# Kernel tuning notes

Measured on AMD Instinct MI355X. Metric: run time of the kernel, lower is better.

Reference implementation:

```python
import jax, jax.numpy as jnp
import numpy as np

B, T = 2, 1000
IN_DIM, OUT_DIM = 257, 514
D_MODEL, D_STATE, D_CONV, EXPAND = 512, 16, 4, 2
D_INNER = EXPAND * D_MODEL          # 1024
DT_RANK = (D_MODEL + 15) // 16      # ceil(512/16) = 32
N_LAYER = 4
K_DC = 31                            # depthwise conv kernel in MambaDCLayer


def layer_norm(x, g, b, eps=1e-5):
    mu = jnp.mean(x, axis=-1, keepdims=True)
    var = jnp.mean((x - mu) ** 2, axis=-1, keepdims=True)
    return (x - mu) * jax.lax.rsqrt(var + eps) * g + b


def dw_conv1d(x, w, b, pad):
    # x: (B, T, C), w: (C, K) depthwise, pad: (left, right)
    y = jax.lax.conv_general_dilated(
        x.transpose(0, 2, 1), w[:, None, :], (1,), [pad],
        dimension_numbers=('NCH', 'OIH', 'NCH'), feature_group_count=w.shape[0])
    return (y + b[None, :, None]).transpose(0, 2, 1)


def mamba_block(x, W_in, conv_w, conv_b, W_x, W_dt, b_dt, A_log, Dp, W_out):
    # x: (B, T, d_model)
    xz = x @ W_in                               # (B, T, 2*D_INNER)
    xin, z = jnp.split(xz, 2, axis=-1)
    xin = dw_conv1d(xin, conv_w, conv_b, (D_CONV - 1, 0))  # causal depthwise conv
    xin = jax.nn.silu(xin)                      # (B, T, D_INNER)
    proj = xin @ W_x                            # (B, T, DT_RANK + 2*D_STATE)
    dt = jax.nn.softplus(proj[..., :DT_RANK] @ W_dt + b_dt)  # (B, T, D_INNER)
    Bm = proj[..., DT_RANK:DT_RANK + D_STATE]   # (B, T, D_STATE)
    Cm = proj[..., DT_RANK + D_STATE:]          # (B, T, D_STATE)
    A = -jnp.exp(A_log)                         # (D_INNER, D_STATE)
    dA = jnp.exp(dt[..., None] * A)             # (B, T, D_INNER, D_STATE)
    dBu = (dt * xin)[..., None] * Bm[:, :, None, :]  # (B, T, D_INNER, D_STATE)

    def step(h, inp):
        dA_t, dBu_t, C_t = inp
        h = dA_t * h + dBu_t
        return h, jnp.einsum('bds,bs->bd', h, C_t)

    h0 = jnp.zeros((x.shape[0], D_INNER, D_STATE), x.dtype)
    _, ys = jax.lax.scan(step, h0, (dA.transpose(1, 0, 2, 3),
                                    dBu.transpose(1, 0, 2, 3),
                                    Cm.transpose(1, 0, 2)))
    y = ys.transpose(1, 0, 2) + xin * Dp        # (B, T, D_INNER)
    y = y * jax.nn.silu(z)
    return y @ W_out                            # (B, T, d_model)


def setup_inputs() -> dict:
    key = jax.random.key(0)
    ks = iter(jax.random.split(key, 32))
    n = lambda shape, s=0.02: jax.random.normal(next(ks), shape, jnp.float32) * s
    return {
        'x': jax.random.normal(next(ks), (B, T, IN_DIM), jnp.float32),
        'lengths': jnp.full((B,), T, jnp.int32),
        'w_in0': n((IN_DIM, D_MODEL)),
        'ln_in_g': jnp.ones((D_MODEL,), jnp.float32),
        'ln_in_b': jnp.zeros((D_MODEL,), jnp.float32),
        'ln1_g': jnp.ones((N_LAYER, D_MODEL), jnp.float32),
        'ln1_b': jnp.zeros((N_LAYER, D_MODEL), jnp.float32),
        'W_inproj': n((N_LAYER, D_MODEL, 2 * D_INNER)),
        'conv_w': n((N_LAYER, D_INNER, D_CONV), 0.1),
        'conv_b': jnp.zeros((N_LAYER, D_INNER), jnp.float32),
        'W_xproj': n((N_LAYER, D_INNER, DT_RANK + 2 * D_STATE)),
        'W_dt': n((N_LAYER, DT_RANK, D_INNER), 0.1),
        'b_dt': jnp.full((N_LAYER, D_INNER), -4.6, jnp.float32),
        'A_log': jnp.tile(jnp.log(jnp.arange(1, D_STATE + 1, dtype=jnp.float32)),
                          (N_LAYER, D_INNER, 1)),
        'D': jnp.ones((N_LAYER, D_INNER), jnp.float32),
        'W_mo': n((N_LAYER, D_INNER, D_MODEL)),
        'ln2_g': jnp.ones((N_LAYER, D_MODEL), jnp.float32),
        'ln2_b': jnp.zeros((N_LAYER, D_MODEL), jnp.float32),
        'dc_w': n((N_LAYER, D_MODEL, K_DC), 0.1),
        'dc_b': jnp.zeros((N_LAYER, D_MODEL), jnp.float32),
        'w_out': n((D_MODEL, OUT_DIM)),
        'b_out': jnp.zeros((OUT_DIM,), jnp.float32),
    }


def reference(x, lengths, w_in0, ln_in_g, ln_in_b, ln1_g, ln1_b, W_inproj,
              conv_w, conv_b, W_xproj, W_dt, b_dt, A_log, D, W_mo,
              ln2_g, ln2_b, dc_w, dc_b, w_out, b_out):
    seq_mask = jnp.arange(x.shape[1]) < lengths[:, None]  # (B, T) bool
    h = jax.nn.relu(layer_norm(x @ w_in0, ln_in_g, ln_in_b))
    for i in range(N_LAYER):
        a = h + mamba_block(layer_norm(h, ln1_g[i], ln1_b[i]),
                            W_inproj[i], conv_w[i], conv_b[i], W_xproj[i],
                            W_dt[i], b_dt[i], A_log[i], D[i], W_mo[i])
        c = dw_conv1d(layer_norm(a, ln2_g[i], ln2_b[i]), dc_w[i], dc_b[i],
                      (K_DC // 2, K_DC // 2))  # 'same' padding
        h = a + c
    out = h @ w_out + b_out  # MagcIRM -> linear output head
    # lengths == T so output[seq_mask] is a full flatten to (B*T, OUT_DIM)
    out_flat = out.reshape(-1, out.shape[-1])
    return out_flat, seq_mask
```

## Files before the change

kernel.cpp:

```cpp
#include <hip/hip_runtime.h>
#include <cstdint>
#include <cstddef>

#define DEVI static __device__ __forceinline__

typedef unsigned short ushort_t;
typedef __attribute__((ext_vector_type(8))) short short8;
typedef __attribute__((ext_vector_type(4))) float f32x4;

DEVI float sp_softplus(float x) { return x > 20.f ? x : log1pf(__expf(x)); }
DEVI float silu_f(float x)      { return x / (1.f + __expf(-x)); }

DEVI ushort_t f2b(float v) {
    uint32_t u = __builtin_bit_cast(uint32_t, v);
    u += 0x7FFFu + ((u >> 16) & 1u);
    return (ushort_t)(u >> 16);
}
DEVI float b2f(ushort_t u) {
    uint32_t x = ((uint32_t)u) << 16;
    return __builtin_bit_cast(float, x);
}

DEVI void gload16(const ushort_t* g, ushort_t* l) {
    __builtin_amdgcn_global_load_lds(
        (const __attribute__((address_space(1))) unsigned int*)g,
        (__attribute__((address_space(3))) unsigned int*)l, 16, 0, 0);
}

#define NC 40
#define CL 25

template<bool RELU, bool OUTB16>
__global__ __launch_bounds__(256) void ln_k(const float* __restrict__ x,
                                            const float* __restrict__ g,
                                            const float* __restrict__ b,
                                            void* __restrict__ yv, int M)
{
    int wid  = threadIdx.x >> 6;
    int lane = threadIdx.x & 63;
    int row  = blockIdx.x * 4 + wid;
    if (row >= M) return;
    const float* xr = x + (size_t)row * 512;
    float4 v0 = *(const float4*)(xr + lane * 8);
    float4 v1 = *(const float4*)(xr + lane * 8 + 4);
    float vals[8] = {v0.x, v0.y, v0.z, v0.w, v1.x, v1.y, v1.z, v1.w};
    float s = 0.f;
#pragma unroll
    for (int i = 0; i < 8; i++) s += vals[i];
#pragma unroll
    for (int off = 1; off < 64; off <<= 1) s += __shfl_xor(s, off);
    float mu = s * (1.f / 512.f);
    float q = 0.f;
#pragma unroll
    for (int i = 0; i < 8; i++) { float d = vals[i] - mu; q += d * d; }
#pragma unroll
    for (int off = 1; off < 64; off <<= 1) q += __shfl_xor(q, off);
    float rstd = rsqrtf(q * (1.f / 512.f) + 1e-5f);
#pragma unroll
    for (int i = 0; i < 8; i++) {
        int c = lane * 8 + i;
        float o = (vals[i] - mu) * rstd * g[c] + b[c];
        if (RELU) o = fmaxf(o, 0.f);
        if (OUTB16) ((ushort_t*)yv)[(size_t)row * 512 + c] = f2b(o);
        else        ((float*)yv)[(size_t)row * 512 + c] = o;
    }
}

__global__ __launch_bounds__(256) void prep_all_k(const float* __restrict__ conv_w,
                                                  const float* __restrict__ dc_w,
                                                  const float* __restrict__ x,
                                                  float* __restrict__ cwt,
                                                  float* __restrict__ dcwt,
                                                  ushort_t* __restrict__ xb)
{
    int e = blockIdx.x * 256 + threadIdx.x;
    if (e < 16384) {
        int l = e >> 12, rem = e & 4095, k = rem >> 10, d = rem & 1023;
        cwt[e] = conv_w[l * 4096 + d * 4 + k];
        return;
    }
    e -= 16384;
    if (e < 63488) {
        int l = e / 15872, rem = e % 15872, k = rem / 512, m = rem % 512;
        dcwt[e] = dc_w[l * 15872 + m * 31 + k];
        return;
    }
    e -= 63488;
    if (e < 2000 * 320) {
        int k = e % 320, row = e / 320;
        xb[e] = (k < 257) ? f2b(x[(size_t)row * 257 + k]) : (ushort_t)0;
    }
}

__global__ __launch_bounds__(256) void tr_w_k(const float* __restrict__ src,
                                              ushort_t* __restrict__ dst,
                                              int Ktrue, int N, int ldo, int srcld,
                                              size_t sstride, size_t dstride)
{
    __shared__ float tile[32][33];
    src += blockIdx.z * sstride;
    dst += blockIdx.z * dstride;
    int n0 = blockIdx.x * 32, k0 = blockIdx.y * 32;
    int tx = threadIdx.x & 31, ty = threadIdx.x >> 5;
#pragma unroll
    for (int r = 0; r < 4; r++) {
        int k = k0 + ty + r * 8, n = n0 + tx;
        tile[ty + r * 8][tx] = (k < Ktrue && n < N) ? src[(size_t)k * srcld + n] : 0.f;
    }
    __syncthreads();
#pragma unroll
    for (int r = 0; r < 4; r++) {
        int n = n0 + ty + r * 8;
        if (n < N) dst[(size_t)n * ldo + k0 + tx] = f2b(tile[tx][ty + r * 8]);
    }
}

template<bool BIAS, int ACT, bool RES, bool OUTF32, bool OUTB16>
__global__ __launch_bounds__(256) void gemm7(
    const ushort_t* __restrict__ A, int lda,
    const ushort_t* __restrict__ Bt, int ldb,
    const float* __restrict__ bias,
    const float* __restrict__ R, int ldr,
    float* __restrict__ C, int ldc,
    ushort_t* __restrict__ C2, int ldc2,
    int M, int N, int K,
    size_t aStr, size_t bStr, size_t cStr)
{
    __shared__ ushort_t As[3 * 4096];
    __shared__ ushort_t Bs[3 * 4096];
    A  += blockIdx.z * aStr;
    Bt += blockIdx.z * bStr;
    C  += blockIdx.z * cStr;
    C2 += blockIdx.z * cStr;

    int tid = threadIdx.x;
    int wid = tid >> 6, l = tid & 63;
    int wr = wid >> 1, wc = wid & 1;
    int lk = l >> 4, lr = l & 15;
    int rhalf = tid >> 3, oct = tid & 7;

    int nwg = gridDim.x * gridDim.y;
    int bid = blockIdx.y * gridDim.x + blockIdx.x;
    {
        int q = nwg >> 3, r = nwg & 7;
        int xcd = bid & 7, lo = bid >> 3;
        bid = (xcd < r ? xcd * (q + 1) : r * (q + 1) + (xcd - r) * q) + lo;
    }
    int bx = bid % gridDim.x, by = bid / gridDim.x;
    int bm = by * 64, bn = bx * 64;

    int cg = oct ^ (rhalf & 7);
    const ushort_t* aS0 = A  + (size_t)(bm + rhalf) * lda + cg * 8;
    const ushort_t* aS1 = aS0 + (size_t)32 * lda;
    const ushort_t* bS0 = Bt + (size_t)(bn + rhalf) * ldb + cg * 8;
    const ushort_t* bS1 = bS0 + (size_t)32 * ldb;

    int rowA = wr * 32 + lr;
    int colB = wc * 32 + lr;
    int a0 = rowA * 64 + ((0 + lk) ^ (rowA & 7)) * 8;
    int a1 = rowA * 64 + ((4 + lk) ^ (rowA & 7)) * 8;
    int b0 = colB * 64 + ((0 + lk) ^ (colB & 7)) * 8;
    int b1 = colB * 64 + ((4 + lk) ^ (colB & 7)) * 8;

    f32x4 acc00 = {0.f,0.f,0.f,0.f}, acc01 = {0.f,0.f,0.f,0.f};
    f32x4 acc10 = {0.f,0.f,0.f,0.f}, acc11 = {0.f,0.f,0.f,0.f};

#define STAGE(B_) do { \
        gload16(aS0, &As[(B_) * 4096 + tid * 8]); \
        gload16(aS1, &As[(B_) * 4096 + 2048 + tid * 8]); \
        gload16(bS0, &Bs[(B_) * 4096 + tid * 8]); \
        gload16(bS1, &Bs[(B_) * 4096 + 2048 + tid * 8]); \
        aS0 += 64; aS1 += 64; bS0 += 64; bS1 += 64; \
    } while (0)

#define COMPUTE(B_) do { \
        short8 af0 = *(const short8*)&As[(B_) * 4096 + a0]; \
        short8 af1 = *(const short8*)&As[(B_) * 4096 + 1024 + a0]; \
        short8 bf0 = *(const short8*)&Bs[(B_) * 4096 + b0]; \
        short8 bf1 = *(const short8*)&Bs[(B_) * 4096 + 1024 + b0]; \
        acc00 = __builtin_amdgcn_mfma_f32_16x16x32_bf16(af0, bf0, acc00, 0, 0, 0); \
        acc01 = __builtin_amdgcn_mfma_f32_16x16x32_bf16(af0, bf1, acc01, 0, 0, 0); \
        acc10 = __builtin_amdgcn_mfma_f32_16x16x32_bf16(af1, bf0, acc10, 0, 0, 0); \
        acc11 = __builtin_amdgcn_mfma_f32_16x16x32_bf16(af1, bf1, acc11, 0, 0, 0); \
        af0 = *(const short8*)&As[(B_) * 4096 + a1]; \
        af1 = *(const short8*)&As[(B_) * 4096 + 1024 + a1]; \
        bf0 = *(const short8*)&Bs[(B_) * 4096 + b1]; \
        bf1 = *(const short8*)&Bs[(B_) * 4096 + 1024 + b1]; \
        acc00 = __builtin_amdgcn_mfma_f32_16x16x32_bf16(af0, bf0, acc00, 0, 0, 0); \
        acc01 = __builtin_amdgcn_mfma_f32_16x16x32_bf16(af0, bf1, acc01, 0, 0, 0); \
        acc10 = __builtin_amdgcn_mfma_f32_16x16x32_bf16(af1, bf0, acc10, 0, 0, 0); \
        acc11 = __builtin_amdgcn_mfma_f32_16x16x32_bf16(af1, bf1, acc11, 0, 0, 0); \
    } while (0)

#define STEP(T_, B_) do { \
        if ((T_) + 1 < nt) asm volatile("s_waitcnt vmcnt(4)" ::: "memory"); \
        else               asm volatile("s_waitcnt vmcnt(0)" ::: "memory"); \
        __builtin_amdgcn_s_barrier(); \
        if ((T_) + 2 < nt) STAGE(((B_) + 2) % 3); \
        COMPUTE(B_); \
    } while (0)

    int nt = K >> 6;
    STAGE(0);
    if (nt > 1) STAGE(1);
    int t = 0;
    for (; t + 3 <= nt; t += 3) { STEP(t, 0); STEP(t + 1, 1); STEP(t + 2, 2); }
    if (t < nt) { STEP(t, 0); t++; }
    if (t < nt) { STEP(t, 1); }

#undef STAGE
#undef COMPUTE
#undef STEP

    f32x4 accs[2][2] = {{acc00, acc01}, {acc10, acc11}};
#pragma unroll
    for (int m = 0; m < 2; m++) {
#pragma unroll
        for (int n = 0; n < 2; n++) {
            int gn = bn + wc * 32 + n * 16 + lr;
            if (gn >= N) continue;
#pragma unroll
            for (int r = 0; r < 4; r++) {
                int gm = bm + wr * 32 + m * 16 + lk * 4 + r;
                if (gm >= M) continue;
                float v = accs[m][n][r];
                if (ACT == 3) {
                    if (gn < 32) C2[(size_t)gm * ldc2 + gn] = f2b(v);
                    else { C[(size_t)gm * ldc + gn] = v;
                           C2[(size_t)gm * ldc2 + gn] = 0; }
                    continue;
                }
                if (BIAS) v += bias[gn];
                if (ACT == 1) v = sp_softplus(v);
                if (RES) v += R[(size_t)gm * ldr + gn];
                if (OUTF32) C[(size_t)gm * ldc + gn] = v;
                if (OUTB16) C2[(size_t)gm * ldc2 + gn] = f2b(v);
            }
        }
    }
}

__global__ __launch_bounds__(256) void conv4_silu_k(const ushort_t* __restrict__ xzb,
                                                    const float* __restrict__ cwt,
                                                    const float* __restrict__ bias,
                                                    ushort_t* __restrict__ xinb)
{
    int e = blockIdx.x * 256 + threadIdx.x;
    if (e >= 2000 * 128) return;
    int dg = (e & 127) * 8;
    int row = e >> 7;
    int b = row >= 1000 ? 1 : 0;
    int t = row - b * 1000;
    float acc[8];
#pragma unroll
    for (int j = 0; j < 8; j++) acc[j] = bias[dg + j];
#pragma unroll
    for (int k = 0; k < 4; k++) {
        int tt = t - 3 + k;
        if (tt < 0) continue;
        short8 v = *(const short8*)&xzb[(size_t)(b * 1000 + tt) * 2048 + dg];
#pragma unroll
        for (int j = 0; j < 8; j++)
            acc[j] += b2f((ushort_t)v[j]) * cwt[k * 1024 + dg + j];
    }
    short8 o;
#pragma unroll
    for (int j = 0; j < 8; j++) o[j] = (short)f2b(silu_f(acc[j]));
    *(short8*)&xinb[(size_t)row * 1024 + dg] = o;
}

__global__ __launch_bounds__(256) void scan_part1(const ushort_t* __restrict__ dt,
                                                  const ushort_t* __restrict__ xin,
                                                  const float* __restrict__ proj,
                                                  const float* __restrict__ A_log,
                                                  float* __restrict__ hloc,
                                                  float* __restrict__ sc)
{
    __shared__ ushort_t s_dt[CL][64], s_x[CL][64];
    __shared__ float s_B[CL][16];
    int d0 = blockIdx.x * 64;
    int c  = blockIdx.y;
    int b  = blockIdx.z;
    int tid = threadIdx.x;
    int ch = tid >> 2, st4 = tid & 3;
    int d = d0 + ch;
    int base = b * 1000 + c * CL;
    for (int lin = tid; lin < CL * 8; lin += 256) {
        int r = lin >> 3, q = lin & 7;
        size_t row = (size_t)(base + r);
        *(short8*)&s_dt[r][q * 8] = *(const short8*)&dt[row * 1024 + d0 + q * 8];
        *(short8*)&s_x[r][q * 8]  = *(const short8*)&xin[row * 1024 + d0 + q * 8];
    }
    for (int lin = tid; lin < CL * 16; lin += 256) {
        int r = lin >> 4, j = lin & 15;
        s_B[r][j] = proj[(size_t)(base + r) * 64 + 32 + j];
    }
    float4 alog = *(const float4*)&A_log[d * 16 + st4 * 4];
    float a_s[4] = {-__expf(alog.x), -__expf(alog.y), -__expf(alog.z), -__expf(alog.w)};
    __syncthreads();
    float h[4] = {0.f, 0.f, 0.f, 0.f};
    float sdt = 0.f;
#pragma unroll 5
    for (int t = 0; t < CL; t++) {
        float dtv = b2f(s_dt[t][ch]);
        float xv  = b2f(s_x[t][ch]);
        float4 Bv = *(const float4*)&s_B[t][st4 * 4];
        float dx = dtv * xv;
        sdt += dtv;
        h[0] = __expf(dtv * a_s[0]) * h[0] + dx * Bv.x;
        h[1] = __expf(dtv * a_s[1]) * h[1] + dx * Bv.y;
        h[2] = __expf(dtv * a_s[2]) * h[2] + dx * Bv.z;
        h[3] = __expf(dtv * a_s[3]) * h[3] + dx * Bv.w;
    }
    *(float4*)&hloc[((size_t)(b * NC + c) << 14) + ((size_t)d << 4) + st4 * 4] =
        (float4){h[0], h[1], h[2], h[3]};
    if (st4 == 0) sc[(b * NC + c) * 1024 + d] = sdt;
}

__global__ __launch_bounds__(256) void scan_combine(const float* __restrict__ A_log,
                                                    float* __restrict__ hloc,
                                                    const float* __restrict__ sc)
{
    int e = blockIdx.x * 256 + threadIdx.x;
    if (e >= 2 * 16384) return;
    int b = e >> 14;
    int rem = e & 16383;
    int dd = rem >> 4;
    float a_s = -__expf(A_log[rem]);
    float H = hloc[((size_t)(b * NC) << 14) + rem];
    for (int c = 1; c < NC; c++) {
        size_t idx = ((size_t)(b * NC + c) << 14) + rem;
        H = hloc[idx] + __expf(a_s * sc[(b * NC + c) * 1024 + dd]) * H;
        hloc[idx] = H;
    }
}

__global__ __launch_bounds__(256) void scan_part2(const ushort_t* __restrict__ dt,
                                                  const ushort_t* __restrict__ xin,
                                                  const float* __restrict__ proj,
                                                  const float* __restrict__ A_log,
                                                  const float* __restrict__ hend,
                                                  const float* __restrict__ Dp,
                                                  const ushort_t* __restrict__ xzb,
                                                  ushort_t* __restrict__ ysb)
{
    __shared__ ushort_t s_dt[CL][64], s_x[CL][64], s_y[CL][64];
    __shared__ float s_B[CL][16], s_C[CL][16];
    __shared__ float s_Dp[64];
    int d0 = blockIdx.x * 64;
    int c  = blockIdx.y;
    int b  = blockIdx.z;
    int tid = threadIdx.x;
    int ch = tid >> 2, st4 = tid & 3;
    int d = d0 + ch;
    int base = b * 1000 + c * CL;
    if (tid < 64) s_Dp[tid] = Dp[d0 + tid];
    for (int lin = tid; lin < CL * 8; lin += 256) {
        int r = lin >> 3, q = lin & 7;
        size_t row = (size_t)(base + r);
        *(short8*)&s_dt[r][q * 8] = *(const short8*)&dt[row * 1024 + d0 + q * 8];
        *(short8*)&s_x[r][q * 8]  = *(const short8*)&xin[row * 1024 + d0 + q * 8];
    }
    for (int lin = tid; lin < CL * 16; lin += 256) {
        int r = lin >> 4, j = lin & 15;
        s_B[r][j] = proj[(size_t)(base + r) * 64 + 32 + j];
        s_C[r][j] = proj[(size_t)(base + r) * 64 + 48 + j];
    }
    float4 alog = *(const float4*)&A_log[d * 16 + st4 * 4];
    float a_s[4] = {-__expf(alog.x), -__expf(alog.y), -__expf(alog.z), -__expf(alog.w)};
    float h[4] = {0.f, 0.f, 0.f, 0.f};
    if (c > 0) {
        float4 hv = *(const float4*)&hend[((size_t)(b * NC + c - 1) << 14)
                                          + ((size_t)d << 4) + st4 * 4];
        h[0] = hv.x; h[1] = hv.y; h[2] = hv.z; h[3] = hv.w;
    }
    __syncthreads();
#pragma unroll 5
    for (int t = 0; t < CL; t++) {
        float dtv = b2f(s_dt[t][ch]);
        float xv  = b2f(s_x[t][ch]);
        float4 Bv = *(const float4*)&s_B[t][st4 * 4];
        float4 Cv = *(const float4*)&s_C[t][st4 * 4];
        float dx = dtv * xv;
        h[0] = __expf(dtv * a_s[0]) * h[0] + dx * Bv.x;
        h[1] = __expf(dtv * a_s[1]) * h[1] + dx * Bv.y;
        h[2] = __expf(dtv * a_s[2]) * h[2] + dx * Bv.z;
        h[3] = __expf(dtv * a_s[3]) * h[3] + dx * Bv.w;
        float p = h[0] * Cv.x + h[1] * Cv.y + h[2] * Cv.z + h[3] * Cv.w;
        p += __shfl_xor(p, 1);
        p += __shfl_xor(p, 2);
        if (st4 == 0) s_y[t][ch] = f2b(p);
    }
    __syncthreads();
    for (int lin = tid; lin < CL * 8; lin += 256) {
        int r = lin >> 3, q = lin & 7;
        size_t row = (size_t)(base + r);
        int dd = d0 + q * 8;
        short8 yv = *(const short8*)&s_y[r][q * 8];
        short8 xv = *(const short8*)&s_x[r][q * 8];
        short8 zv = *(const short8*)&xzb[row * 2048 + 1024 + dd];
        short8 ov;
#pragma unroll
        for (int j = 0; j < 8; j++) {
            float o = (b2f((ushort_t)yv[j]) + b2f((ushort_t)xv[j]) * s_Dp[q * 8 + j])
                      * silu_f(b2f((ushort_t)zv[j]));
            ov[j] = (short)f2b(o);
        }
        *(short8*)&ysb[row * 1024 + dd] = ov;
    }
}

template<bool FUSE_LN>
__global__ __launch_bounds__(256) void dcconv_ln_k(
    const ushort_t* __restrict__ ln, const float* __restrict__ a,
    const float* __restrict__ dcwt, const float* __restrict__ bias,
    const float* __restrict__ g, const float* __restrict__ bb,
    float* __restrict__ h, ushort_t* __restrict__ out)
{
    __shared__ float red[8];
    int row = blockIdx.x;
    int b = row >= 1000 ? 1 : 0;
    int t = row - b * 1000;
    int tid = threadIdx.x;
    int m0 = tid * 2;
    float acc0 = bias[m0], acc1 = bias[m0 + 1];
#pragma unroll
    for (int k = 0; k < 31; k++) {
        int tt = t - 15 + k;
        if (tt >= 0 && tt < 1000) {
            uint32_t v = *(const uint32_t*)&ln[(size_t)(b * 1000 + tt) * 512 + m0];
            float2 w = *(const float2*)&dcwt[k * 512 + m0];
            acc0 += b2f((ushort_t)(v & 0xffff)) * w.x;
            acc1 += b2f((ushort_t)(v >> 16)) * w.y;
        }
    }
    float2 avv = *(const float2*)&a[(size_t)row * 512 + m0];
    float v0 = avv.x + acc0, v1 = avv.y + acc1;
    *(float2*)&h[(size_t)row * 512 + m0] = (float2){v0, v1};
    if (!FUSE_LN) {
        uint32_t o = (uint32_t)f2b(v0) | ((uint32_t)f2b(v1) << 16);
        *(uint32_t*)&out[(size_t)row * 512 + m0] = o;
        return;
    }
    int wv = tid >> 6, lane = tid & 63;
    float s = v0 + v1;
#pragma unroll
    for (int off = 1; off < 64; off <<= 1) s += __shfl_xor(s, off);
    if (lane == 0) red[wv] = s;
    __syncthreads();
    float mu = (red[0] + red[1] + red[2] + red[3]) * (1.f / 512.f);
    float q = (v0 - mu) * (v0 - mu) + (v1 - mu) * (v1 - mu);
#pragma unroll
    for (int off = 1; off < 64; off <<= 1) q += __shfl_xor(q, off);
    if (lane == 0) red[4 + wv] = q;
    __syncthreads();
    float var = (red[4] + red[5] + red[6] + red[7]) * (1.f / 512.f);
    float rstd = rsqrtf(var + 1e-5f);
    uint32_t o = (uint32_t)f2b((v0 - mu) * rstd * g[m0] + bb[m0])
               | ((uint32_t)f2b((v1 - mu) * rstd * g[m0 + 1] + bb[m0 + 1]) << 16);
    *(uint32_t*)&out[(size_t)row * 512 + m0] = o;
}

__global__ void mask_k(const int* __restrict__ lengths, float* __restrict__ out)
{
    int i = blockIdx.x * 256 + threadIdx.x;
    if (i >= 2000) return;
    out[i] = ((i % 1000) < lengths[i / 1000]) ? 1.f : 0.f;
}

extern "C" void kernel_launch(void* const* d_in, const int* in_sizes, int n_in,
                              void* d_out, int out_size, void* d_ws, size_t ws_size,
                              hipStream_t stream)
{
    const float* x       = (const float*)d_in[0];
    const int*   lengths = (const int*)  d_in[1];
    const float* w_in0   = (const float*)d_in[2];
    const float* ln_in_g = (const float*)d_in[3];
    const float* ln_in_b = (const float*)d_in[4];
    const float* ln1_g   = (const float*)d_in[5];
    const float* ln1_b   = (const float*)d_in[6];
    const float* W_inproj= (const float*)d_in[7];
    const float* conv_w  = (const float*)d_in[8];
    const float* conv_b  = (const float*)d_in[9];
    const float* W_xproj = (const float*)d_in[10];
    const float* W_dt    = (const float*)d_in[11];
    const float* b_dt    = (const float*)d_in[12];
    const float* A_log   = (const float*)d_in[13];
    const float* Dp      = (const float*)d_in[14];
    const float* W_mo    = (const float*)d_in[15];
    const float* ln2_g   = (const float*)d_in[16];
    const float* ln2_b   = (const float*)d_in[17];
    const float* dc_w    = (const float*)d_in[18];
    const float* dc_b    = (const float*)d_in[19];
    const float* w_out   = (const float*)d_in[20];
    const float* b_out   = (const float*)d_in[21];

    char* p = (char*)d_ws;
    auto alloc_f = [&](size_t n) { float* r = (float*)p; p += n * 4; return r; };
    auto alloc_b = [&](size_t n) { ushort_t* r = (ushort_t*)p; p += n * 2; return r; };

    float* h    = alloc_f(2048 * 512);
    float* lnb  = alloc_f(2048 * 512);
    float* proj = alloc_f(2048 * 64);
    float* av   = alloc_f(2048 * 512);
    float* hloc = alloc_f((size_t)2 * NC * 16384);
    float* sc   = alloc_f((size_t)2 * NC * 1024);
    float* cwt  = alloc_f(4 * 4 * 1024);
    float* dcwt = alloc_f(4 * 31 * 512);
    ushort_t* xbf   = alloc_b(2048 * 320);
    ushort_t* lnbb  = alloc_b(2048 * 512);
    ushort_t* lnc   = alloc_b(2048 * 512);
    ushort_t* xzb   = alloc_b(2048 * 2048);
    ushort_t* xinb  = alloc_b(2048 * 1024);
    ushort_t* dtbb  = alloc_b(2048 * 1024);
    ushort_t* ysb   = alloc_b(2048 * 1024);
    ushort_t* hb    = alloc_b(2048 * 512);
    ushort_t* projb = alloc_b(2048 * 64);
    ushort_t* wt_in0 = alloc_b(512 * 320);
    ushort_t* wt_in  = alloc_b((size_t)4 * 2048 * 512);
    ushort_t* wt_dt  = alloc_b((size_t)4 * 1024 * 64);
    ushort_t* wt_mo  = alloc_b((size_t)4 * 512 * 1024);
    ushort_t* wt_out = alloc_b(576 * 512);
    ushort_t* wxt    = alloc_b((size_t)4 * 64 * 1024);

    dim3 blk(256);

    prep_all_k<<<(16384 + 63488 + 2000 * 320 + 255) / 256, blk, 0, stream>>>(
        conv_w, dc_w, x, cwt, dcwt, xbf);
    tr_w_k<<<dim3(16, 10, 1), blk, 0, stream>>>(w_in0, wt_in0, 257, 512, 320, 512, 0, 0);
    tr_w_k<<<dim3(64, 16, 4), blk, 0, stream>>>(W_inproj, wt_in, 512, 2048, 512, 2048,
                                                (size_t)512 * 2048, (size_t)2048 * 512);
    tr_w_k<<<dim3(32, 2, 4),  blk, 0, stream>>>(W_dt, wt_dt, 32, 1024, 64, 1024,
                                                (size_t)32 * 1024, (size_t)1024 * 64);
    tr_w_k<<<dim3(16, 32, 4), blk, 0, stream>>>(W_mo, wt_mo, 1024, 512, 1024, 512,
                                                (size_t)1024 * 512, (size_t)512 * 1024);
    tr_w_k<<<dim3(17, 16, 1), blk, 0, stream>>>(w_out, wt_out, 512, 514, 512, 514, 0, 0);
    tr_w_k<<<dim3(2, 32, 4),  blk, 0, stream>>>(W_xproj, wxt, 1024, 64, 1024, 64,
                                                (size_t)1024 * 64, (size_t)64 * 1024);

    gemm7<false, 0, false, true, false><<<dim3(8, 32), blk, 0, stream>>>(
        xbf, 320, wt_in0, 320, nullptr, nullptr, 0, lnb, 512, nullptr, 0,
        2000, 512, 320, 0, 0, 0);
    ln_k<true, false><<<500, blk, 0, stream>>>(lnb, ln_in_g, ln_in_b, h, 2000);
    ln_k<false, true><<<500, blk, 0, stream>>>(h, ln1_g, ln1_b, lnbb, 2000);

    for (int i = 0; i < 4; i++) {
        const float* Al = A_log + (size_t)i * 16384;
        gemm7<false, 0, false, false, true><<<dim3(32, 32), blk, 0, stream>>>(
            lnbb, 512, wt_in + (size_t)i * 2048 * 512, 512,
            nullptr, nullptr, 0, nullptr, 0, xzb, 2048, 2000, 2048, 512, 0, 0, 0);
        conv4_silu_k<<<1000, blk, 0, stream>>>(xzb, cwt + i * 4096,
                                               conv_b + i * 1024, xinb);
        gemm7<false, 3, false, false, false><<<dim3(1, 32), blk, 0, stream>>>(
            xinb, 1024, wxt + (size_t)i * 64 * 1024, 1024,
            nullptr, nullptr, 0, proj, 64, projb, 64, 2000, 64, 1024, 0, 0, 0);
        gemm7<true, 1, false, false, true><<<dim3(16, 32), blk, 0, stream>>>(
            projb, 64, wt_dt + (size_t)i * 1024 * 64, 64,
            b_dt + i * 1024, nullptr, 0, nullptr, 0, dtbb, 1024,
            2000, 1024, 64, 0, 0, 0);
        scan_part1<<<dim3(16, NC, 2), blk, 0, stream>>>(dtbb, xinb, proj, Al, hloc, sc);
        scan_combine<<<128, blk, 0, stream>>>(Al, hloc, sc);
        scan_part2<<<dim3(16, NC, 2), blk, 0, stream>>>(dtbb, xinb, proj, Al, hloc,
                                                        Dp + i * 1024, xzb, ysb);
        gemm7<false, 0, true, true, false><<<dim3(8, 32), blk, 0, stream>>>(
            ysb, 1024, wt_mo + (size_t)i * 512 * 1024, 1024,
            nullptr, h, 512, av, 512, nullptr, 0, 2000, 512, 1024, 0, 0, 0);
        ln_k<false, true><<<500, blk, 0, stream>>>(av, ln2_g + i * 512, ln2_b + i * 512,
                                                   lnc, 2000);
        if (i < 3)
            dcconv_ln_k<true><<<2000, blk, 0, stream>>>(
                lnc, av, dcwt + i * 31 * 512, dc_b + i * 512,
                ln1_g + (i + 1) * 512, ln1_b + (i + 1) * 512, h, lnbb);
        else
            dcconv_ln_k<false><<<2000, blk, 0, stream>>>(
                lnc, av, dcwt + i * 31 * 512, dc_b + i * 512,
                nullptr, nullptr, h, hb);
    }

    gemm7<true, 0, false, true, false><<<dim3(9, 32), blk, 0, stream>>>(
        hb, 512, wt_out, 512, b_out, nullptr, 0, (float*)d_out, 514, nullptr, 0,
        2000, 514, 512, 0, 0, 0);
    mask_k<<<8, blk, 0, stream>>>(lengths, (float*)d_out + 2000 * 514);
}
```

Baseline: 474.1 us.

## Fuse causal conv, x-projection and dt-projection into one per-row kernel

Replaces the conv4+SiLU kernel, the x_proj GEMM and the dt_proj GEMM with a single per-row kernel. It keeps xin in shared memory, computes the 64-wide projection with CUDA-core dot products, then the dt projection plus softplus directly from fp32 W_dt. It also merges the two initial LayerNorm kernels into one. This removes three launches per layer and the intermediate round trips through global memory. The cost is that the matmuls drop from MFMA to scalar FMA, and each row block re-reads the weight matrices.

```diff
diff --git a/kernel.cpp b/kernel.cpp
--- a/kernel.cpp
+++ b/kernel.cpp
@@ -63,6 +63,60 @@
         if (RELU) o = fmaxf(o, 0.f);
         if (OUTB16) ((ushort_t*)yv)[(size_t)row * 512 + c] = f2b(o);
         else        ((float*)yv)[(size_t)row * 512 + c] = o;
+    }
+}
+
+__global__ __launch_bounds__(256) void ln2x_k(const float* __restrict__ x,
+                                              const float* __restrict__ g0,
+                                              const float* __restrict__ b0,
+                                              const float* __restrict__ g1,
+                                              const float* __restrict__ b1,
+                                              float* __restrict__ h,
+                                              ushort_t* __restrict__ lnbb, int M)
+{
+    int wid  = threadIdx.x >> 6;
+    int lane = threadIdx.x & 63;
+    int row  = blockIdx.x * 4 + wid;
+    if (row >= M) return;
+    const float* xr = x + (size_t)row * 512;
+    float4 v0 = *(const float4*)(xr + lane * 8);
+    float4 v1 = *(const float4*)(xr + lane * 8 + 4);
+    float vals[8] = {v0.x, v0.y, v0.z, v0.w, v1.x, v1.y, v1.z, v1.w};
+    float s = 0.f;
+#pragma unroll
+    for (int i = 0; i < 8; i++) s += vals[i];
+#pragma unroll
+    for (int off = 1; off < 64; off <<= 1) s += __shfl_xor(s, off);
+    float mu = s * (1.f / 512.f);
+    float q = 0.f;
+#pragma unroll
+    for (int i = 0; i < 8; i++) { float d = vals[i] - mu; q += d * d; }
+#pragma unroll
+    for (int off = 1; off < 64; off <<= 1) q += __shfl_xor(q, off);
+    float rstd = rsqrtf(q * (1.f / 512.f) + 1e-5f);
+    float o[8];
+#pragma unroll
+    for (int i = 0; i < 8; i++) {
+        int c = lane * 8 + i;
+        o[i] = fmaxf((vals[i] - mu) * rstd * g0[c] + b0[c], 0.f);
+        h[(size_t)row * 512 + c] = o[i];
+    }
+    float s2 = 0.f;
+#pragma unroll
+    for (int i = 0; i < 8; i++) s2 += o[i];
+#pragma unroll
+    for (int off = 1; off < 64; off <<= 1) s2 += __shfl_xor(s2, off);
+    float mu2 = s2 * (1.f / 512.f);
+    float q2 = 0.f;
+#pragma unroll
+    for (int i = 0; i < 8; i++) { float d = o[i] - mu2; q2 += d * d; }
+#pragma unroll
+    for (int off = 1; off < 64; off <<= 1) q2 += __shfl_xor(q2, off);
+    float rstd2 = rsqrtf(q2 * (1.f / 512.f) + 1e-5f);
+#pragma unroll
+    for (int i = 0; i < 8; i++) {
+        int c = lane * 8 + i;
+        lnbb[(size_t)row * 512 + c] = f2b((o[i] - mu2) * rstd2 * g1[c] + b1[c]);
     }
 }
 
@@ -224,12 +278,6 @@
                 int gm = bm + wr * 32 + m * 16 + lk * 4 + r;
                 if (gm >= M) continue;
                 float v = accs[m][n][r];
-                if (ACT == 3) {
-                    if (gn < 32) C2[(size_t)gm * ldc2 + gn] = f2b(v);
-                    else { C[(size_t)gm * ldc + gn] = v;
-                           C2[(size_t)gm * ldc2 + gn] = 0; }
-                    continue;
-                }
                 if (BIAS) v += bias[gn];
                 if (ACT == 1) v = sp_softplus(v);
                 if (RES) v += R[(size_t)gm * ldr + gn];
@@ -240,33 +288,75 @@
     }
 }
 
-__global__ __launch_bounds__(256) void conv4_silu_k(const ushort_t* __restrict__ xzb,
-                                                    const float* __restrict__ cwt,
-                                                    const float* __restrict__ bias,
-                                                    ushort_t* __restrict__ xinb)
-{
-    int e = blockIdx.x * 256 + threadIdx.x;
-    if (e >= 2000 * 128) return;
-    int dg = (e & 127) * 8;
-    int row = e >> 7;
+__global__ __launch_bounds__(256) void midfuse_k(
+    const ushort_t* __restrict__ xzb, const float* __restrict__ cwt,
+    const float* __restrict__ conv_b, const ushort_t* __restrict__ wxt,
+    const float* __restrict__ W_dt, const float* __restrict__ b_dt,
+    ushort_t* __restrict__ xinb, float* __restrict__ proj,
+    ushort_t* __restrict__ dtbb)
+{
+    __shared__ float s_xin[1024];
+    __shared__ float s_proj[64];
+    int row = blockIdx.x;
     int b = row >= 1000 ? 1 : 0;
     int t = row - b * 1000;
-    float acc[8];
-#pragma unroll
-    for (int j = 0; j < 8; j++) acc[j] = bias[dg + j];
+    int tid = threadIdx.x;
+    int dg = tid * 4;
+
+    float4 cb = *(const float4*)&conv_b[dg];
+    float acc[4] = {cb.x, cb.y, cb.z, cb.w};
 #pragma unroll
     for (int k = 0; k < 4; k++) {
         int tt = t - 3 + k;
         if (tt < 0) continue;
-        short8 v = *(const short8*)&xzb[(size_t)(b * 1000 + tt) * 2048 + dg];
-#pragma unroll
-        for (int j = 0; j < 8; j++)
-            acc[j] += b2f((ushort_t)v[j]) * cwt[k * 1024 + dg + j];
-    }
-    short8 o;
-#pragma unroll
-    for (int j = 0; j < 8; j++) o[j] = (short)f2b(silu_f(acc[j]));
-    *(short8*)&xinb[(size_t)row * 1024 + dg] = o;
+        uint2 v = *(const uint2*)&xzb[(size_t)(b * 1000 + tt) * 2048 + dg];
+        float4 w = *(const float4*)&cwt[k * 1024 + dg];
+        acc[0] += b2f((ushort_t)(v.x & 0xffff)) * w.x;
+        acc[1] += b2f((ushort_t)(v.x >> 16))    * w.y;
+        acc[2] += b2f((ushort_t)(v.y & 0xffff)) * w.z;
+        acc[3] += b2f((ushort_t)(v.y >> 16))    * w.w;
+    }
+    uint32_t ou[4];
+#pragma unroll
+    for (int j = 0; j < 4; j++) {
+        ou[j] = f2b(silu_f(acc[j]));
+        s_xin[dg + j] = b2f((ushort_t)ou[j]);
+    }
+    uint2 xw = {ou[0] | (ou[1] << 16), ou[2] | (ou[3] << 16)};
+    *(uint2*)&xinb[(size_t)row * 1024 + dg] = xw;
+    __syncthreads();
+
+    int j = tid >> 2, sub = tid & 3;
+    const ushort_t* wrow = wxt + (size_t)j * 1024 + sub * 256;
+    const float* xrow = s_xin + sub * 256;
+    float p = 0.f;
+#pragma unroll 4
+    for (int i = 0; i < 256; i += 8) {
+        short8 w = *(const short8*)&wrow[i];
+#pragma unroll
+        for (int e = 0; e < 8; e++) p += xrow[i + e] * b2f((ushort_t)w[e]);
+    }
+    p += __shfl_xor(p, 1);
+    p += __shfl_xor(p, 2);
+    if (sub == 0) {
+        s_proj[j] = p;
+        proj[(size_t)row * 64 + j] = p;
+    }
+    __syncthreads();
+
+    float4 bd = *(const float4*)&b_dt[dg];
+    float da[4] = {bd.x, bd.y, bd.z, bd.w};
+#pragma unroll 8
+    for (int k = 0; k < 32; k++) {
+        float pk = s_proj[k];
+        float4 w = *(const float4*)&W_dt[k * 1024 + dg];
+        da[0] += pk * w.x; da[1] += pk * w.y; da[2] += pk * w.z; da[3] += pk * w.w;
+    }
+    uint32_t du[4];
+#pragma unroll
+    for (int q = 0; q < 4; q++) du[q] = f2b(sp_softplus(da[q]));
+    uint2 dw = {du[0] | (du[1] << 16), du[2] | (du[3] << 16)};
+    *(uint2*)&dtbb[(size_t)row * 1024 + dg] = dw;
 }
 
 __global__ __launch_bounds__(256) void scan_part1(const ushort_t* __restrict__ dt,
@@ -515,10 +605,8 @@
     ushort_t* dtbb  = alloc_b(2048 * 1024);
     ushort_t* ysb   = alloc_b(2048 * 1024);
     ushort_t* hb    = alloc_b(2048 * 512);
-    ushort_t* projb = alloc_b(2048 * 64);
     ushort_t* wt_in0 = alloc_b(512 * 320);
     ushort_t* wt_in  = alloc_b((size_t)4 * 2048 * 512);
-    ushort_t* wt_dt  = alloc_b((size_t)4 * 1024 * 64);
     ushort_t* wt_mo  = alloc_b((size_t)4 * 512 * 1024);
     ushort_t* wt_out = alloc_b(576 * 512);
     ushort_t* wxt    = alloc_b((size_t)4 * 64 * 1024);
@@ -530,8 +618,6 @@
     tr_w_k<<<dim3(16, 10, 1), blk, 0, stream>>>(w_in0, wt_in0, 257, 512, 320, 512, 0, 0);
     tr_w_k<<<dim3(64, 16, 4), blk, 0, stream>>>(W_inproj, wt_in, 512, 2048, 512, 2048,
                                                 (size_t)512 * 2048, (size_t)2048 * 512);
-    tr_w_k<<<dim3(32, 2, 4),  blk, 0, stream>>>(W_dt, wt_dt, 32, 1024, 64, 1024,
-                                                (size_t)32 * 1024, (size_t)1024 * 64);
     tr_w_k<<<dim3(16, 32, 4), blk, 0, stream>>>(W_mo, wt_mo, 1024, 512, 1024, 512,
                                                 (size_t)1024 * 512, (size_t)512 * 1024);
     tr_w_k<<<dim3(17, 16, 1), blk, 0, stream>>>(w_out, wt_out, 512, 514, 512, 514, 0, 0);
@@ -541,23 +627,16 @@
     gemm7<false, 0, false, true, false><<<dim3(8, 32), blk, 0, stream>>>(
         xbf, 320, wt_in0, 320, nullptr, nullptr, 0, lnb, 512, nullptr, 0,
         2000, 512, 320, 0, 0, 0);
-    ln_k<true, false><<<500, blk, 0, stream>>>(lnb, ln_in_g, ln_in_b, h, 2000);
-    ln_k<false, true><<<500, blk, 0, stream>>>(h, ln1_g, ln1_b, lnbb, 2000);
+    ln2x_k<<<500, blk, 0, stream>>>(lnb, ln_in_g, ln_in_b, ln1_g, ln1_b, h, lnbb, 2000);
 
     for (int i = 0; i < 4; i++) {
         const float* Al = A_log + (size_t)i * 16384;
         gemm7<false, 0, false, false, true><<<dim3(32, 32), blk, 0, stream>>>(
             lnbb, 512, wt_in + (size_t)i * 2048 * 512, 512,
             nullptr, nullptr, 0, nullptr, 0, xzb, 2048, 2000, 2048, 512, 0, 0, 0);
-        conv4_silu_k<<<1000, blk, 0, stream>>>(xzb, cwt + i * 4096,
-                                               conv_b + i * 1024, xinb);
-        gemm7<false, 3, false, false, false><<<dim3(1, 32), blk, 0, stream>>>(
-            xinb, 1024, wxt + (size_t)i * 64 * 1024, 1024,
-            nullptr, nullptr, 0, proj, 64, projb, 64, 2000, 64, 1024, 0, 0, 0);
-        gemm7<true, 1, false, false, true><<<dim3(16, 32), blk, 0, stream>>>(
-            projb, 64, wt_dt + (size_t)i * 1024 * 64, 64,
-            b_dt + i * 1024, nullptr, 0, nullptr, 0, dtbb, 1024,
-            2000, 1024, 64, 0, 0, 0);
+        midfuse_k<<<2000, blk, 0, stream>>>(
+            xzb, cwt + i * 4096, conv_b + i * 1024, wxt + (size_t)i * 64 * 1024,
+            W_dt + (size_t)i * 32 * 1024, b_dt + i * 1024, xinb, proj, dtbb);
         scan_part1<<<dim3(16, NC, 2), blk, 0, stream>>>(dtbb, xinb, proj, Al, hloc, sc);
         scan_combine<<<128, blk, 0, stream>>>(Al, hloc, sc);
         scan_part2<<<dim3(16, NC, 2), blk, 0, stream>>>(dtbb, xinb, proj, Al, hloc,
```

Measured after the change: 533.5 us. +12.5%, slower.
